# Optimization experiments

Measured on AMD Instinct MI355X. Metric: run time of the kernel, lower is better.

## Reference

```python
import jax, jax.numpy as jnp
import numpy as np
import math

N_HEADS = 16
ROPE_THETA = 10000.0
NEG_INF = -1e30


def setup_inputs() -> dict:
    key = jax.random.key(0)
    k1, k2, k3, k4 = jax.random.split(key, 4)
    B, S, D = 2, 2048, 2048
    x = jax.random.normal(k1, (B, S, D), dtype=jnp.float32)
    qkv = 0.01 * jax.random.normal(k2, (2 * D, D), dtype=jnp.float32)
    H = N_HEADS
    dh = D // H
    nope = dh // 2
    rope = dh // 2
    wk = 0.01 * jax.random.normal(k3, (H * nope + rope, D), dtype=jnp.float32)
    wo = 0.01 * jax.random.normal(k4, (D, D), dtype=jnp.float32)
    return {"x": x, "qkv": qkv, "wk": wk, "wo": wo}


def _rope_cos_sin(S, dh, rope_dim, dtype):
    # freqs over full dh as in the torch module, then sliced to rope_dim//2 and tiled x2
    freqs = 1.0 / (ROPE_THETA ** (jnp.arange(0, dh, 2).astype(jnp.float32) / dh))
    emb = jnp.arange(S, dtype=jnp.float32)[:, None] * freqs[None, :]  # [S, dh//2]
    cos = jnp.tile(jnp.cos(emb)[:, : rope_dim // 2], (1, 2))[None, None]  # [1,1,S,rope]
    sin = jnp.tile(jnp.sin(emb)[:, : rope_dim // 2], (1, 2))[None, None]
    return cos.astype(dtype), sin.astype(dtype)


def _apply_rope(xq, cos, sin):
    x1, x2 = jnp.split(xq, 2, axis=-1)
    return xq * cos + jnp.concatenate([-x2, x1], axis=-1) * sin


def reference(x, qkv, wk, wo):
    B, S, D = x.shape
    H = N_HEADS
    dh = D // H
    nope = dh // 2
    rope = dh // 2

    QV = x @ qkv.T                              # [B,S,2D]
    Q, V = jnp.split(QV, 2, axis=-1)
    Q = Q.reshape(B, S, H, dh).transpose(0, 2, 1, 3)        # [B,H,S,dh]
    v_heads = V.reshape(B, S, H, dh).transpose(0, 2, 1, 3)  # [B,H,S,dh]
    Qn, Qr = Q[..., :nope], Q[..., nope:]

    K = x @ wk.T                                # [B,S,H*nope+rope]
    Kn = K[..., : H * nope].reshape(B, S, H, nope).transpose(0, 2, 1, 3)  # [B,H,S,nope]
    Kr = K[..., H * nope :].reshape(B, S, 1, rope).transpose(0, 2, 1, 3)  # [B,1,S,rope]

    cos, sin = _rope_cos_sin(S, dh, rope, x.dtype)
    Qr = _apply_rope(Qr, cos, sin)
    Kr = _apply_rope(Kr, cos, sin)

    q_heads = jnp.concatenate([Qn, Qr], axis=-1)                               # [B,H,S,dh]
    k_heads = jnp.concatenate([Kn, jnp.broadcast_to(Kr, (B, H, S, rope))], -1)  # [B,H,S,dh]

    scale = 1.0 / math.sqrt(dh)
    scores = jnp.einsum('bhqd,bhkd->bhqk', q_heads, k_heads) * scale
    mask = jnp.tril(jnp.ones((S, S), dtype=bool))
    scores = jnp.where(mask[None, None], scores, NEG_INF)
    attn = jax.nn.softmax(scores, axis=-1)
    out = jnp.einsum('bhqk,bhkd->bhqd', attn, v_heads)
    out = out.transpose(0, 2, 1, 3).reshape(B, S, D) @ wo.T
    return (out, k_heads, v_heads)
```

## Files before the change

kernel.cpp:

```cpp
#include <hip/hip_runtime.h>
#include <hip/hip_bf16.h>


typedef unsigned short u16;
typedef unsigned int u32;
typedef __bf16 bf16x8 __attribute__((ext_vector_type(8)));
typedef float f32x4 __attribute__((ext_vector_type(4)));

__device__ __forceinline__ u16 f2bf(float x) {
  union { __hip_bfloat16 h; u16 u; } c;
  c.h = __float2bfloat16(x);
  return c.u;
}
__device__ __forceinline__ float bf2f(u16 u) {
  union { u32 u; float f; } c;
  c.u = ((u32)u) << 16;
  return c.f;
}
__device__ __forceinline__ f32x4 mfma16(bf16x8 a, bf16x8 b, f32x4 c) {
  return __builtin_amdgcn_mfma_f32_16x16x32_bf16(a, b, c, 0, 0, 0);
}
__device__ __forceinline__ void gload_lds16(const void* g, void* l) {
  __builtin_amdgcn_global_load_lds((__attribute__((address_space(1))) void*)g,
                                   (__attribute__((address_space(3))) void*)l,
                                   16, 0, 0);
}

__global__ __launch_bounds__(256) void cast_all(const float4* __restrict__ x,
                                                const float4* __restrict__ qkv,
                                                const float* __restrict__ wk,
                                                const float4* __restrict__ wo,
                                                u16* __restrict__ x_bf,
                                                u16* __restrict__ wcomb,
                                                u16* __restrict__ wo_bf) {
  int i = blockIdx.x * blockDim.x + threadIdx.x;
  const float4* src;
  u16* dst;
  int j;
  if (i < 2097152) {
    src = x; dst = x_bf; j = i;
  } else if (i < 4194304) {
    src = qkv; dst = wcomb; j = i - 2097152;
  } else if (i < 4849664) {
    j = i - 4194304;
    int r = (j * 4) >> 11;
    u32 lo = 0, hi = 0;
    if (r < 1088) {
      float4 v = ((const float4*)wk)[j];
      lo = (u32)f2bf(v.x) | ((u32)f2bf(v.y) << 16);
      hi = (u32)f2bf(v.z) | ((u32)f2bf(v.w) << 16);
    }
    ((uint2*)(wcomb + 8388608))[j] = make_uint2(lo, hi);
    return;
  } else {
    src = wo; dst = wo_bf; j = i - 4849664;
  }
  float4 v = src[j];
  u32 lo = (u32)f2bf(v.x) | ((u32)f2bf(v.y) << 16);
  u32 hi = (u32)f2bf(v.z) | ((u32)f2bf(v.w) << 16);
  ((uint2*)dst)[j] = make_uint2(lo, hi);
}

__device__ __forceinline__ void cstore(u16* C, size_t i, float v) { C[i] = f2bf(v); }
__device__ __forceinline__ void cstore(float* C, size_t i, float v) { C[i] = v; }

template <typename CT, int BM>
__global__ __launch_bounds__(512, 2) void gemm256(const u16* __restrict__ A,
                                                  const u16* __restrict__ W,
                                                  CT* __restrict__ C,
                                                  int M, int N, int K) {
  constexpr int MI = BM / 64;
  constexpr int AH = BM * 64;
  constexpr int AL = BM / 128;
  constexpr int BOFF = 4 * AH;
  __shared__ char lds[BOFF + 65536];
  const int tid = threadIdx.x;
  const int wid = tid >> 6, lane = tid & 63;
  const int lr = lane & 15, lg = lane >> 4;
  const int wr = wid >> 2, wc = wid & 3;
  const int xorv = (lr & 7) << 4;
  const int nwg = gridDim.x * gridDim.y;
  const int lin = blockIdx.y * gridDim.x + blockIdx.x;
  const int swz = (lin & 7) * (nwg >> 3) + (lin >> 3);
  const int m0 = (swz / gridDim.x) * BM;
  const int n0 = (swz % gridDim.x) * 256;
  const int nkt = K >> 6;

  f32x4 acc[2 * MI][4] = {};
  bf16x8 a[MI][2], b[4][2];

  const int o0 = tid * 16, o1 = 8192 + tid * 16;
  const int r0 = o0 >> 7, c0 = ((o0 & 127) ^ ((r0 & 7) << 4)) >> 1;
  const int r1 = o1 >> 7, c1 = ((o1 & 127) ^ ((r1 & 7) << 4)) >> 1;
  const u16* gA0[2] = {A + (size_t)(m0 + r0) * K + c0,
                       A + (size_t)(m0 + BM / 2 + r0) * K + c0};
  const u16* gA1[2] = {A + (size_t)(m0 + r1) * K + c1,
                       A + (size_t)(m0 + BM / 2 + r1) * K + c1};
  const u16* gB0[2] = {W + (size_t)(n0 + r0) * K + c0,
                       W + (size_t)(n0 + 128 + r0) * K + c0};
  const u16* gB1[2] = {W + (size_t)(n0 + r1) * K + c1,
                       W + (size_t)(n0 + 128 + r1) * K + c1};

  auto STAGEA = [&](int t, int h) {
    char* d_ = lds + (t & 1) * (2 * AH) + h * AH + wid * 1024;
    gload_lds16(gA0[h] + (size_t)t * 64, d_);
    if constexpr (AL == 2) gload_lds16(gA1[h] + (size_t)t * 64, d_ + 8192);
  };
  auto STAGEB = [&](int t, int h) {
    char* d_ = lds + BOFF + (t & 1) * 32768 + h * 16384 + wid * 1024;
    gload_lds16(gB0[h] + (size_t)t * 64, d_);
    gload_lds16(gB1[h] + (size_t)t * 64, d_ + 8192);
  };
  auto WAITKEEP = [&]() {
    if constexpr (BM == 256) asm volatile("s_waitcnt vmcnt(4)" ::: "memory");
    else asm volatile("s_waitcnt vmcnt(3)" ::: "memory");
  };

  STAGEA(0, 0); STAGEB(0, 0); STAGEA(0, 1); STAGEB(0, 1);
  if (nkt > 1) { STAGEA(1, 0); STAGEB(1, 0); }
  WAITKEEP();
  __builtin_amdgcn_s_barrier();

  for (int t = 0; t < nkt; ++t) {
    const char* Ab = lds + (t & 1) * (2 * AH);
    const char* Bb = lds + BOFF + (t & 1) * 32768;
    const int arow = wr * (BM / 4), brow = wc * 32;
#pragma unroll
    for (int mi = 0; mi < MI; mi++)
#pragma unroll
      for (int ks = 0; ks < 2; ks++)
        a[mi][ks] = *(const bf16x8*)(Ab + (arow + mi * 16 + lr) * 128 + ((lg * 16 + ks * 64) ^ xorv));
#pragma unroll
    for (int ni = 0; ni < 2; ni++)
#pragma unroll
      for (int ks = 0; ks < 2; ks++)
        b[ni][ks] = *(const bf16x8*)(Bb + (brow + ni * 16 + lr) * 128 + ((lg * 16 + ks * 64) ^ xorv));
    if (t + 1 < nkt) STAGEA(t + 1, 1);
    __builtin_amdgcn_s_barrier();
    asm volatile("s_waitcnt lgkmcnt(0)" ::: "memory");
    __builtin_amdgcn_sched_barrier(0);
    __builtin_amdgcn_s_setprio(1);
#pragma unroll
    for (int mi = 0; mi < MI; mi++)
#pragma unroll
      for (int ni = 0; ni < 2; ni++)
#pragma unroll
        for (int ks = 0; ks < 2; ks++)
          acc[mi][ni] = mfma16(a[mi][ks], b[ni][ks], acc[mi][ni]);
    __builtin_amdgcn_s_setprio(0);
    __builtin_amdgcn_s_barrier();
#pragma unroll
    for (int ni = 0; ni < 2; ni++)
#pragma unroll
      for (int ks = 0; ks < 2; ks++)
        b[2 + ni][ks] = *(const bf16x8*)(Bb + 16384 + (brow + ni * 16 + lr) * 128 + ((lg * 16 + ks * 64) ^ xorv));
    if (t + 1 < nkt) STAGEB(t + 1, 1);
    __builtin_amdgcn_s_barrier();
    asm volatile("s_waitcnt lgkmcnt(0)" ::: "memory");
    __builtin_amdgcn_sched_barrier(0);
    __builtin_amdgcn_s_setprio(1);
#pragma unroll
    for (int mi = 0; mi < MI; mi++)
#pragma unroll
      for (int ni = 0; ni < 2; ni++)
#pragma unroll
        for (int ks = 0; ks < 2; ks++)
          acc[mi][2 + ni] = mfma16(a[mi][ks], b[2 + ni][ks], acc[mi][2 + ni]);
    __builtin_amdgcn_s_setprio(0);
    __builtin_amdgcn_s_barrier();
#pragma unroll
    for (int mi = 0; mi < MI; mi++)
#pragma unroll
      for (int ks = 0; ks < 2; ks++)
        a[mi][ks] = *(const bf16x8*)(Ab + AH + (arow + mi * 16 + lr) * 128 + ((lg * 16 + ks * 64) ^ xorv));
    if (t + 2 < nkt) STAGEA(t + 2, 0);
    __builtin_amdgcn_s_barrier();
    asm volatile("s_waitcnt lgkmcnt(0)" ::: "memory");
    __builtin_amdgcn_sched_barrier(0);
    __builtin_amdgcn_s_setprio(1);
#pragma unroll
    for (int mi = 0; mi < MI; mi++)
#pragma unroll
      for (int ni = 0; ni < 2; ni++)
#pragma unroll
        for (int ks = 0; ks < 2; ks++)
          acc[MI + mi][ni] = mfma16(a[mi][ks], b[ni][ks], acc[MI + mi][ni]);
    __builtin_amdgcn_s_setprio(0);
    __builtin_amdgcn_s_barrier();
    if (t + 2 < nkt) {
      STAGEB(t + 2, 0);
      WAITKEEP();
    } else if (t + 1 < nkt) {
      asm volatile("s_waitcnt vmcnt(0)" ::: "memory");
    }
    __builtin_amdgcn_s_barrier();
    asm volatile("s_waitcnt lgkmcnt(0)" ::: "memory");
    __builtin_amdgcn_sched_barrier(0);
    __builtin_amdgcn_s_setprio(1);
#pragma unroll
    for (int mi = 0; mi < MI; mi++)
#pragma unroll
      for (int ni = 0; ni < 2; ni++)
#pragma unroll
        for (int ks = 0; ks < 2; ks++)
          acc[MI + mi][2 + ni] = mfma16(a[mi][ks], b[2 + ni][ks], acc[MI + mi][2 + ni]);
    __builtin_amdgcn_s_setprio(0);
    __builtin_amdgcn_s_barrier();
  }

#pragma unroll
  for (int Mh = 0; Mh < 2; Mh++)
#pragma unroll
    for (int mi = 0; mi < MI; mi++) {
      int row = m0 + Mh * (BM / 2) + wr * (BM / 4) + mi * 16 + lg * 4;
#pragma unroll
      for (int Nh = 0; Nh < 2; Nh++)
#pragma unroll
        for (int ni = 0; ni < 2; ni++) {
          int col = n0 + Nh * 128 + wc * 32 + ni * 16 + lr;
#pragma unroll
          for (int r = 0; r < 4; r++)
            cstore(C, (size_t)(row + r) * N + col, acc[Mh * MI + mi][Nh * 2 + ni][r]);
        }
    }
}

__global__ __launch_bounds__(256) void rope_scatter2(u16* __restrict__ QVK,
                                                     u16* __restrict__ kh,
                                                     float* __restrict__ k_out, int S) {
  const int row = blockIdx.x;
  const int b = row >> 11, s = row & 2047;
  const int tid = threadIdx.x;
  __shared__ float kr[64];
  const float LOG1E4_64 = 0.14391156511f;
  u16* qrow = QVK + (size_t)row * 5376;
  if (tid < 32) {
    float freq = __expf(-(float)tid * LOG1E4_64);
    float sn, c;
    __sincosf((float)s * freq, &sn, &c);
    float a = bf2f(qrow[5120 + tid]);
    float bb = bf2f(qrow[5152 + tid]);
    kr[tid] = a * c - bb * sn;
    kr[tid + 32] = bb * c + a * sn;
  }
  for (int idx = tid; idx < 512; idx += 256) {
    int h = idx >> 5, jj = idx & 31;
    float freq = __expf(-(float)jj * LOG1E4_64);
    float sn, c;
    __sincosf((float)s * freq, &sn, &c);
    u16* p1 = qrow + h * 128 + 64 + jj;
    u16* p2 = qrow + h * 128 + 96 + jj;
    float x1 = bf2f(*p1), x2 = bf2f(*p2);
    *p1 = f2bf(x1 * c - x2 * sn);
    *p2 = f2bf(x2 * c + x1 * sn);
  }
  __syncthreads();
  for (int idx = tid; idx < 2048; idx += 256) {
    int h = idx >> 7, d = idx & 127;
    float val = (d < 64) ? bf2f(qrow[4096 + h * 64 + d]) : kr[d - 64];
    size_t o = ((size_t)(b * 16 + h) * S + s) * 128 + d;
    kh[o] = f2bf(val);
    k_out[o] = val;
  }
}

__global__ __launch_bounds__(256) void v_scatter(const u16* __restrict__ QVK,
                                                 u16* __restrict__ vt,
                                                 float* __restrict__ v_out, int S) {
  const int blk = blockIdx.x;
  const int st = blk & 63;
  const int dt = (blk >> 6) & 3;
  const int bh = blk >> 8;
  const int b = bh >> 4, h = bh & 15;
  __shared__ u16 t[32][34];
  const int tx = threadIdx.x & 31, ty = threadIdx.x >> 5;
  const int s0 = st * 32, d0 = dt * 32;
#pragma unroll
  for (int i = 0; i < 4; i++) {
    int sl = ty + 8 * i;
    u16 u = QVK[(size_t)(b * S + s0 + sl) * 5376 + 2048 + h * 128 + d0 + tx];
    t[sl][tx] = u;
    v_out[((size_t)bh * S + s0 + sl) * 128 + d0 + tx] = bf2f(u);
  }
  __syncthreads();
#pragma unroll
  for (int i = 0; i < 4; i++) {
    int dl = ty + 8 * i;
    vt[((size_t)bh * 128 + d0 + dl) * S + s0 + tx] = t[tx][dl];
  }
}

__global__ __launch_bounds__(256) void flash_attn2(const u16* __restrict__ QVK,
                                                   const u16* __restrict__ Kh,
                                                   const u16* __restrict__ Vt,
                                                   u16* __restrict__ attn, int S) {
  __shared__ char lds[65536];
  const int tid = threadIdx.x, wid = tid >> 6, lane = tid & 63;
  const int bh = blockIdx.x & 31;
  const int qb = 31 - (int)(blockIdx.x >> 5);
  const int q0 = qb * 64 + wid * 16;
  const int b = bh >> 4, h = bh & 15;
  const int q = lane & 15, g = lane >> 4;
  const u16* Qb = QVK + (size_t)b * S * 5376 + h * 128;
  const u16* Kb = Kh + (size_t)bh * S * 128;
  const u16* Vb = Vt + (size_t)bh * 128 * S;
  const int qg = q0 + q;
  const int xr = (q & 7) << 4;

  const u16* srcK[4];
  const u16* srcV[4];
#pragma unroll
  for (int i = 0; i < 4; i++) {
    int o = ((i * 4 + wid) << 10) | (lane << 4);
    int rK = o >> 8, cbK = (o & 255) ^ ((rK & 7) << 4);
    srcK[i] = Kb + rK * 128 + (cbK >> 1);
    int dV = o >> 7, kbV = (o & 127) ^ ((dV & 7) << 4);
    srcV[i] = Vb + (size_t)dV * S + (kbV >> 1);
  }

  bf16x8 qf[4];
#pragma unroll
  for (int f = 0; f < 4; f++)
    qf[f] = *(const bf16x8*)(Qb + (size_t)qg * 5376 + f * 32 + g * 8);

  f32x4 acc[8] = {};
  float m = -INFINITY, l = 0.f;
  const float sc = 0.08838834764831845f;
  const int ktiles = qb + 1;

#pragma unroll
  for (int i = 0; i < 4; i++) {
    char* ld = lds + ((i * 4 + wid) << 10);
    gload_lds16(srcK[i], ld);
    gload_lds16(srcV[i], ld + 32768);
  }
  asm volatile("s_waitcnt vmcnt(0)" ::: "memory");
  __syncthreads();

  int buf = 0;
  for (int kt = 0; kt < ktiles; ++kt) {
    if (kt + 1 < ktiles) {
      const int nb = buf ^ 1;
      const int adv = (kt + 1) * 8192;
      const int advv = (kt + 1) * 64;
#pragma unroll
      for (int i = 0; i < 4; i++) {
        char* ld = lds + nb * 16384 + ((i * 4 + wid) << 10);
        gload_lds16(srcK[i] + adv, ld);
        gload_lds16(srcV[i] + advv, ld + 32768);
      }
    }
    const char* Kt = lds + buf * 16384;
    const char* Vl = lds + 32768 + buf * 16384;

    f32x4 s[4] = {};
    const char* Kq = Kt + q * 256;
    __builtin_amdgcn_s_setprio(1);
#pragma unroll
    for (int f = 0; f < 4; f++) {
#pragma unroll
      for (int c = 0; c < 4; c++) {
        bf16x8 kf = *(const bf16x8*)(Kq + c * 4096 + ((f * 64 + g * 16) ^ xr));
        s[c] = mfma16(kf, qf[f], s[c]);
      }
    }
    __builtin_amdgcn_s_setprio(0);

    const int kbg = kt * 64;
    float v[16];
    const bool maskt = (kbg + 63 > q0);
#pragma unroll
    for (int c = 0; c < 4; c++)
#pragma unroll
      for (int r = 0; r < 4; r++) {
        float x = s[c][r];
        if (maskt && (kbg + c * 16 + g * 4 + r > qg)) x = -1e30f;
        v[c * 4 + r] = x;
      }
    float tm = v[0];
#pragma unroll
    for (int i = 1; i < 16; i++) tm = fmaxf(tm, v[i]);
    tm = fmaxf(tm, __shfl_xor(tm, 16));
    tm = fmaxf(tm, __shfl_xor(tm, 32));
    if (!__all(tm <= m + 64.0f)) {
      float mnew = fmaxf(m, tm);
      float corr = __expf((m - mnew) * sc);
      m = mnew;
      l *= corr;
      float corr_r[4];
#pragma unroll
      for (int r = 0; r < 4; r++)
        corr_r[r] = __shfl(corr, (lane & 48) | (g * 4 + r));
#pragma unroll
      for (int j = 0; j < 8; j++)
#pragma unroll
        for (int r = 0; r < 4; r++) acc[j][r] *= corr_r[r];
    }
    const float nms = -m * sc;
    float p[16], ts = 0.f;
#pragma unroll
    for (int i = 0; i < 16; i++) {
      p[i] = __expf(fmaf(v[i], sc, nms));
      ts += p[i];
    }
    ts += __shfl_xor(ts, 16);
    ts += __shfl_xor(ts, 32);
    l += ts;

    const int src0 = q | ((g & 1) << 5);
    const bool hi = (g & 2);
    union { u32 u[4]; bf16x8 v; } pcA, pcB;
    {
      u32 w0a = (u32)f2bf(p[0]) | ((u32)f2bf(p[1]) << 16);
      u32 w0b = (u32)f2bf(p[2]) | ((u32)f2bf(p[3]) << 16);
      u32 w1a = (u32)f2bf(p[4]) | ((u32)f2bf(p[5]) << 16);
      u32 w1b = (u32)f2bf(p[6]) | ((u32)f2bf(p[7]) << 16);
      u32 a_lo  = (u32)__shfl((int)w0a, src0);
      u32 b_lo  = (u32)__shfl((int)w0b, src0);
      u32 a_lo2 = (u32)__shfl((int)w0a, src0 + 16);
      u32 b_lo2 = (u32)__shfl((int)w0b, src0 + 16);
      u32 a_hi  = (u32)__shfl((int)w1a, src0);
      u32 b_hi  = (u32)__shfl((int)w1b, src0);
      u32 a_hi2 = (u32)__shfl((int)w1a, src0 + 16);
      u32 b_hi2 = (u32)__shfl((int)w1b, src0 + 16);
      pcA.u[0] = hi ? a_hi : a_lo;
      pcA.u[1] = hi ? b_hi : b_lo;
      pcA.u[2] = hi ? a_hi2 : a_lo2;
      pcA.u[3] = hi ? b_hi2 : b_lo2;
    }
    {
      u32 w0a = (u32)f2bf(p[8])  | ((u32)f2bf(p[9])  << 16);
      u32 w0b = (u32)f2bf(p[10]) | ((u32)f2bf(p[11]) << 16);
      u32 w1a = (u32)f2bf(p[12]) | ((u32)f2bf(p[13]) << 16);
      u32 w1b = (u32)f2bf(p[14]) | ((u32)f2bf(p[15]) << 16);
      u32 a_lo  = (u32)__shfl((int)w0a, src0);
      u32 b_lo  = (u32)__shfl((int)w0b, src0);
      u32 a_lo2 = (u32)__shfl((int)w0a, src0 + 16);
      u32 b_lo2 = (u32)__shfl((int)w0b, src0 + 16);
      u32 a_hi  = (u32)__shfl((int)w1a, src0);
      u32 b_hi  = (u32)__shfl((int)w1b, src0);
      u32 a_hi2 = (u32)__shfl((int)w1a, src0 + 16);
      u32 b_hi2 = (u32)__shfl((int)w1b, src0 + 16);
      pcB.u[0] = hi ? a_hi : a_lo;
      pcB.u[1] = hi ? b_hi : b_lo;
      pcB.u[2] = hi ? a_hi2 : a_lo2;
      pcB.u[3] = hi ? b_hi2 : b_lo2;
    }
    const int vcolA = (g * 16) ^ xr;
    const int vcolB = (64 + g * 16) ^ xr;
    __builtin_amdgcn_s_setprio(1);
#pragma unroll
    for (int j = 0; j < 8; j++) {
      bf16x8 vfA = *(const bf16x8*)(Vl + (j * 16 + q) * 128 + vcolA);
      acc[j] = mfma16(pcA.v, vfA, acc[j]);
    }
#pragma unroll
    for (int j = 0; j < 8; j++) {
      bf16x8 vfB = *(const bf16x8*)(Vl + (j * 16 + q) * 128 + vcolB);
      acc[j] = mfma16(pcB.v, vfB, acc[j]);
    }
    __builtin_amdgcn_s_setprio(0);

    asm volatile("s_waitcnt vmcnt(0)" ::: "memory");
    __syncthreads();
    buf ^= 1;
  }

  float linv = 1.0f / l;
  float linv_r[4];
#pragma unroll
  for (int r = 0; r < 4; r++)
    linv_r[r] = __shfl(linv, (lane & 48) | (g * 4 + r));
  u16* ab = attn + (size_t)(b * S + q0) * 2048 + h * 128;
#pragma unroll
  for (int j = 0; j < 8; j++)
#pragma unroll
    for (int r = 0; r < 4; r++)
      ab[(size_t)(g * 4 + r) * 2048 + j * 16 + q] = f2bf(acc[j][r] * linv_r[r]);
}

extern "C" void kernel_launch(void* const* d_in, const int* in_sizes, int n_in,
                              void* d_out, int out_size, void* d_ws, size_t ws_size,
                              hipStream_t stream) {
  (void)in_sizes; (void)n_in; (void)out_size; (void)ws_size;
  const int S = 2048;
  const float* x = (const float*)d_in[0];
  const float* qkv = (const float*)d_in[1];
  const float* wk = (const float*)d_in[2];
  const float* wo = (const float*)d_in[3];
  float* out = (float*)d_out;
  float* k_out = out + (size_t)8388608;
  float* v_out = out + (size_t)16777216;

  char* ws = (char*)d_ws;
  u16* x_bf  = (u16*)(ws + 0);
  u16* wcomb = (u16*)(ws + 16777216);
  u16* wo_bf = (u16*)(ws + 38797312);
  u16* qvk   = (u16*)(ws + 47185920);
  u16* vt_bf = (u16*)(ws + 91226112);
  u16* attn_bf = x_bf;
  u16* k_bf = wcomb;

  cast_all<<<23040, 256, 0, stream>>>((const float4*)x, (const float4*)qkv, wk,
                                      (const float4*)wo, x_bf, wcomb, wo_bf);

  gemm256<u16, 256><<<dim3(21, 16), 512, 0, stream>>>(x_bf, wcomb, qvk, 4096, 5376, 2048);
  rope_scatter2<<<4096, 256, 0, stream>>>(qvk, k_bf, k_out, S);
  v_scatter<<<8192, 256, 0, stream>>>(qvk, vt_bf, v_out, S);
  flash_attn2<<<1024, 256, 0, stream>>>(qvk, k_bf, vt_bf, attn_bf, S);
  gemm256<float, 128><<<dim3(8, 32), 512, 0, stream>>>(attn_bf, wo_bf, out, 4096, 2048, 2048);
}
```

Before: 289.3 us.

## Use 128-query flash-attention blocks with 8 waves and split K/V LDS staging

The attention kernel goes from 4 to 8 waves per block, so each block covers 128 queries and each K/V tile loaded into LDS is reused by twice as many queries. K stays double-buffered while V uses a single buffer that is refilled after the PV MFMAs, with finer vmcnt waits and raw s_barrier calls, which cuts LDS to 48KB. The QKV projection GEMM also switches to a 128-wide tile with twice as many blocks. The costs are fewer attention blocks (512), more barriers per tile, and V loads that are less overlapped.

New measurement: 287.2 us. No clear change (-0.8%).

```diff
diff --git a/kernel.cpp b/kernel.cpp
--- a/kernel.cpp
+++ b/kernel.cpp
@@ -290,15 +290,15 @@
   }
 }
 
-__global__ __launch_bounds__(256) void flash_attn2(const u16* __restrict__ QVK,
+__global__ __launch_bounds__(512) void flash_attn3(const u16* __restrict__ QVK,
                                                    const u16* __restrict__ Kh,
                                                    const u16* __restrict__ Vt,
                                                    u16* __restrict__ attn, int S) {
-  __shared__ char lds[65536];
+  __shared__ char lds[49152];
   const int tid = threadIdx.x, wid = tid >> 6, lane = tid & 63;
   const int bh = blockIdx.x & 31;
-  const int qb = 31 - (int)(blockIdx.x >> 5);
-  const int q0 = qb * 64 + wid * 16;
+  const int qb = 15 - (int)(blockIdx.x >> 5);
+  const int q0 = qb * 128 + wid * 16;
   const int b = bh >> 4, h = bh & 15;
   const int q = lane & 15, g = lane >> 4;
   const u16* Qb = QVK + (size_t)b * S * 5376 + h * 128;
@@ -307,11 +307,11 @@
   const int qg = q0 + q;
   const int xr = (q & 7) << 4;
 
-  const u16* srcK[4];
-  const u16* srcV[4];
-#pragma unroll
-  for (int i = 0; i < 4; i++) {
-    int o = ((i * 4 + wid) << 10) | (lane << 4);
+  const u16* srcK[2];
+  const u16* srcV[2];
+#pragma unroll
+  for (int i = 0; i < 2; i++) {
+    int o = ((i * 8 + wid) << 10) | (lane << 4);
     int rK = o >> 8, cbK = (o & 255) ^ ((rK & 7) << 4);
     srcK[i] = Kb + rK * 128 + (cbK >> 1);
     int dV = o >> 7, kbV = (o & 127) ^ ((dV & 7) << 4);
@@ -326,32 +326,31 @@
   f32x4 acc[8] = {};
   float m = -INFINITY, l = 0.f;
   const float sc = 0.08838834764831845f;
-  const int ktiles = qb + 1;
-
-#pragma unroll
-  for (int i = 0; i < 4; i++) {
-    char* ld = lds + ((i * 4 + wid) << 10);
+  const int ktiles = 2 * qb + 2;
+
+#pragma unroll
+  for (int i = 0; i < 2; i++) {
+    char* ld = lds + ((i * 8 + wid) << 10);
     gload_lds16(srcK[i], ld);
     gload_lds16(srcV[i], ld + 32768);
   }
   asm volatile("s_waitcnt vmcnt(0)" ::: "memory");
-  __syncthreads();
-
-  int buf = 0;
+  __builtin_amdgcn_s_barrier();
+
   for (int kt = 0; kt < ktiles; ++kt) {
-    if (kt + 1 < ktiles) {
-      const int nb = buf ^ 1;
-      const int adv = (kt + 1) * 8192;
-      const int advv = (kt + 1) * 64;
-#pragma unroll
-      for (int i = 0; i < 4; i++) {
-        char* ld = lds + nb * 16384 + ((i * 4 + wid) << 10);
-        gload_lds16(srcK[i] + adv, ld);
-        gload_lds16(srcV[i] + advv, ld + 32768);
-      }
-    }
-    const char* Kt = lds + buf * 16384;
-    const char* Vl = lds + 32768 + buf * 16384;
+    const char* Kt = lds + (kt & 1) * 16384;
+    const char* Vl = lds + 32768;
+    const bool more = (kt + 1 < ktiles);
+    if (more) {
+#pragma unroll
+      for (int i = 0; i < 2; i++)
+        gload_lds16(srcK[i] + (size_t)(kt + 1) * 8192,
+                    lds + (((kt & 1) ^ 1) << 14) + ((i * 8 + wid) << 10));
+      asm volatile("s_waitcnt vmcnt(4)" ::: "memory");
+    } else {
+      asm volatile("s_waitcnt vmcnt(2)" ::: "memory");
+    }
+    __builtin_amdgcn_s_barrier();
 
     f32x4 s[4] = {};
     const char* Kq = Kt + q * 256;
@@ -446,6 +445,11 @@
       pcB.u[2] = hi ? a_hi2 : a_lo2;
       pcB.u[3] = hi ? b_hi2 : b_lo2;
     }
+
+    if (more) asm volatile("s_waitcnt vmcnt(2)" ::: "memory");
+    else      asm volatile("s_waitcnt vmcnt(0)" ::: "memory");
+    __builtin_amdgcn_s_barrier();
+
     const int vcolA = (g * 16) ^ xr;
     const int vcolB = (64 + g * 16) ^ xr;
     __builtin_amdgcn_s_setprio(1);
@@ -461,9 +465,13 @@
     }
     __builtin_amdgcn_s_setprio(0);
 
-    asm volatile("s_waitcnt vmcnt(0)" ::: "memory");
-    __syncthreads();
-    buf ^= 1;
+    __builtin_amdgcn_s_barrier();
+    if (more) {
+#pragma unroll
+      for (int i = 0; i < 2; i++)
+        gload_lds16(srcV[i] + (size_t)(kt + 1) * 64,
+                    lds + 32768 + ((i * 8 + wid) << 10));
+    }
   }
 
   float linv = 1.0f / l;
@@ -504,9 +512,9 @@
   cast_all<<<23040, 256, 0, stream>>>((const float4*)x, (const float4*)qkv, wk,
                                       (const float4*)wo, x_bf, wcomb, wo_bf);
 
-  gemm256<u16, 256><<<dim3(21, 16), 512, 0, stream>>>(x_bf, wcomb, qvk, 4096, 5376, 2048);
+  gemm256<u16, 128><<<dim3(21, 32), 512, 0, stream>>>(x_bf, wcomb, qvk, 4096, 5376, 2048);
   rope_scatter2<<<4096, 256, 0, stream>>>(qvk, k_bf, k_out, S);
   v_scatter<<<8192, 256, 0, stream>>>(qvk, vt_bf, v_out, S);
-  flash_attn2<<<1024, 256, 0, stream>>>(qvk, k_bf, vt_bf, attn_bf, S);
+  flash_attn3<<<512, 512, 0, stream>>>(qvk, k_bf, vt_bf, attn_bf, S);
   gemm256<float, 128><<<dim3(8, 32), 512, 0, stream>>>(attn_bf, wo_bf, out, 4096, 2048, 2048);
 }
```
